# Optimization experiments

Hardware: AMD Instinct MI355X
Metric: run time of the kernel (lower is better)

The kernel has to match this reference:

```python
import jax, jax.numpy as jnp
import numpy as np

NUM_LOW, NUM_HIGH, DIM = 8192, 1024, 2048
EPS = 1e-10


def sparsemax(z):
    # z: [..., K]; Martins & Astudillo sparsemax along last axis.
    K = z.shape[-1]
    z_sorted = jnp.flip(jnp.sort(z, axis=-1), axis=-1)          # descending
    z_cum = jnp.cumsum(z_sorted, axis=-1)
    k = jnp.arange(1, K + 1, dtype=z.dtype)
    support = (1.0 + k * z_sorted) > z_cum                       # bool [..., K]
    k_sup = jnp.sum(support, axis=-1, keepdims=True)             # int [..., 1]
    tau = (jnp.take_along_axis(z_cum, k_sup - 1, axis=-1) - 1.0) / k_sup.astype(z.dtype)
    return jnp.maximum(z - tau, 0.0)


def normalize_rows(x, eps=EPS):
    return x / (jnp.sum(x, axis=1, keepdims=True) + eps)


def setup_inputs() -> dict:
    key = jax.random.key(0)
    k1, k2, k3, k4 = jax.random.split(key, 4)

    def xavier(k, shape):
        bound = float(np.sqrt(6.0 / (shape[0] + shape[1])))
        return jax.random.uniform(k, shape, jnp.float32, -bound, bound)

    return {
        "low_w": xavier(k1, (NUM_LOW, DIM)),    # low Concepts parameter
        "high_w": xavier(k2, (NUM_HIGH, DIM)),  # high Concepts parameter
        "Wq": xavier(k3, (DIM, DIM)),           # q_linear.weight (keep_head_dim, n_head=1)
        "Wk": xavier(k4, (DIM, DIM)),           # k_linear.weight
        "norm_low_concepts": 1,
        "norm_high_concepts": 1,
    }


def reference(low_w, high_w, Wq, Wk, norm_low_concepts, norm_high_concepts):
    # Concepts modules: return (possibly normalized) concepts + cosine similarity.
    low_normed = low_w / jnp.linalg.norm(low_w, axis=1, keepdims=True)
    low_concepts = low_normed if norm_low_concepts else low_w
    low_cos = low_normed @ low_normed.T                          # [NL, NL]

    high_normed = high_w / jnp.linalg.norm(high_w, axis=1, keepdims=True)
    high_concepts = high_normed if norm_high_concepts else high_w
    high_cos = high_normed @ high_normed.T                       # [NH, NH]

    # detach_low_concepts=True -> queries do not receive gradients
    low_q = jax.lax.stop_gradient(low_concepts)

    # ModifiedMultiHeadAttention (n_head=1, keep_head_dim -> d_head=DIM; eval mode,
    # so smooth_max is identity and sparsemax is deterministic).
    q = low_q @ Wq.T                                             # [NL, D]
    k = high_concepts @ Wk.T                                     # [NH, D]
    scale = 1.0 / jnp.sqrt(jnp.asarray(DIM, q.dtype))
    attn = sparsemax((q @ k.T) * scale)                          # [NL, NH]
    high_related_low = attn @ high_concepts                      # [NL, D]

    # output_high_concepts_type == "high_plus_low": add back aggregated low concepts
    aggregated_low = normalize_rows(attn.T) @ low_q              # [NH, D]
    output_high_concepts = high_related_low + attn @ aggregated_low  # [NL, D]

    return (low_concepts, low_cos, output_high_concepts, high_cos, attn)
```

## Files before the change

### kernel.cpp

```cpp
#include <hip/hip_runtime.h>
#include <hip/hip_bf16.h>
#include <stdint.h>

#define NL   8192
#define NHI  1024
#define DIMV 2048

typedef __attribute__((ext_vector_type(8))) short short8;
typedef __attribute__((ext_vector_type(4))) float f32x4;

__device__ __forceinline__ unsigned short f2bf(float x){
  unsigned u = __float_as_uint(x);
  u += 0x7FFFu + ((u >> 16) & 1u);
  return (unsigned short)(u >> 16);
}
__device__ __forceinline__ float bf2f(unsigned short b){
  return __uint_as_float(((unsigned)b) << 16);
}
__device__ __forceinline__ unsigned pack2bf(float a, float b){
  return (unsigned)f2bf(a) | ((unsigned)f2bf(b) << 16);
}

__device__ __forceinline__ void gload16(const void* g, void* l){
  __builtin_amdgcn_global_load_lds(
      (const __attribute__((address_space(1))) unsigned int*)g,
      (__attribute__((address_space(3))) unsigned int*)l, 16, 0, 0);
}

__global__ __launch_bounds__(256)
void prep_kernel(const float* __restrict__ low_w, const float* __restrict__ high_w,
                 const float* __restrict__ Wq, const float* __restrict__ Wk,
                 float* __restrict__ out_lowc, unsigned short* __restrict__ lowN,
                 unsigned short* __restrict__ highN,
                 unsigned short* __restrict__ WqB, unsigned short* __restrict__ WkB){
  int id = blockIdx.x;
  if(id < 9216){
    const float* W; float* oF; unsigned short* oB; int row;
    if(id < 8192){ W = low_w; oF = out_lowc; oB = lowN; row = id; }
    else         { W = high_w; oF = nullptr; oB = highN; row = id - 8192; }
    const float* r = W + (size_t)row * DIMV;
    int base = threadIdx.x * 8;
    float4 x0 = *(const float4*)(r + base);
    float4 x1 = *(const float4*)(r + base + 4);
    float ss = x0.x*x0.x + x0.y*x0.y + x0.z*x0.z + x0.w*x0.w
             + x1.x*x1.x + x1.y*x1.y + x1.z*x1.z + x1.w*x1.w;
    #pragma unroll
    for(int s = 1; s < 64; s <<= 1) ss += __shfl_xor(ss, s, 64);
    __shared__ float red[4];
    if((threadIdx.x & 63) == 0) red[threadIdx.x >> 6] = ss;
    __syncthreads();
    float tot = red[0] + red[1] + red[2] + red[3];
    float inv = 1.0f / sqrtf(tot);
    float y0=x0.x*inv, y1=x0.y*inv, y2=x0.z*inv, y3=x0.w*inv;
    float y4=x1.x*inv, y5=x1.y*inv, y6=x1.z*inv, y7=x1.w*inv;
    if(oF){
      float* o = oF + (size_t)row * DIMV + base;
      *(float4*)o       = make_float4(y0,y1,y2,y3);
      *(float4*)(o + 4) = make_float4(y4,y5,y6,y7);
    }
    uint4 u;
    u.x = pack2bf(y0,y1); u.y = pack2bf(y2,y3);
    u.z = pack2bf(y4,y5); u.w = pack2bf(y6,y7);
    *(uint4*)(oB + (size_t)row * DIMV + base) = u;
  } else {
    id -= 9216;
    const float* in; unsigned short* outp;
    if(id < 2048){ in = Wq; outp = WqB; } else { in = Wk; outp = WkB; id -= 2048; }
    size_t i = ((size_t)id * 256 + threadIdx.x) * 8;
    float4 x0 = *(const float4*)(in + i);
    float4 x1 = *(const float4*)(in + i + 4);
    uint4 u;
    u.x = pack2bf(x0.x,x0.y); u.y = pack2bf(x0.z,x0.w);
    u.z = pack2bf(x1.x,x1.y); u.w = pack2bf(x1.z,x1.w);
    *(uint4*)(outp + i) = u;
  }
}

template<int OUT_BF16, int MIRROR>
__global__ __launch_bounds__(256, 2)
void gemm_bt_kernel(const unsigned short* __restrict__ A,
                    const unsigned short* __restrict__ Bt,
                    float* __restrict__ Cf, unsigned short* __restrict__ Cb,
                    int M, int N, int K, float scale){
  __shared__ __align__(16) char smem[32768];
  unsigned short* sA = (unsigned short*)smem;
  unsigned short* sB = sA + 128 * 64;

  int tid = threadIdx.x, lane = tid & 63, wid = tid >> 6;
  int mBase, nBase;
  if(MIRROR){
    int orig = blockIdx.x;
    int id = (orig & 7) * 260 + (orig >> 3);
    int Si = 0, rem = id;
    for(;;){ int rl = 10 + 16*(15 - Si); if(rem < rl) break; rem -= rl; Si++; }
    int bi, bj;
    if(rem < 10){
      int ti = 0;
      while((ti+1)*4 - (((ti+1)*ti) >> 1) <= rem) ti++;
      int off = ti*4 - ((ti*(ti-1)) >> 1);
      int tj = ti + (rem - off);
      bi = Si*4 + ti; bj = Si*4 + tj;
    } else {
      int r2 = rem - 10;
      int Sj = Si + 1 + (r2 >> 4);
      int t = r2 & 15;
      bi = Si*4 + (t >> 2); bj = Sj*4 + (t & 3);
    }
    mBase = bi * 128; nBase = bj * 128;
  } else {
    int gx = gridDim.x, gy = gridDim.y;
    int nwg = gx * gy;
    int id = blockIdx.y * gx + blockIdx.x;
    if((nwg & 7) == 0){ int cpx = nwg >> 3; id = (id & 7) * cpx + (id >> 3); }
    mBase = (id / gx) * 128; nBase = (id % gx) * 128;
  }

  int chRow = lane >> 3;
  int chCol = (lane & 7) * 8;
  int wm = wid >> 1, wn = wid & 1;

  f32x4 acc[4][4];
  #pragma unroll
  for(int i=0;i<4;i++)
    #pragma unroll
    for(int j=0;j<4;j++) acc[i][j] = (f32x4){0.f,0.f,0.f,0.f};

  int kChunk = K / (int)gridDim.z;
  int kStart = kChunk * (int)blockIdx.z;
  if(!OUT_BF16) Cf += (size_t)blockIdx.z * M * N;

  for(int k0 = kStart; k0 < kStart + kChunk; k0 += 64){
    #pragma unroll
    for(int i = 0; i < 4; i++){
      int ch = wid * 4 + i;
      int arow = ch * 8 + chRow;
      gload16(A  + (size_t)(mBase + arow) * K + k0 + chCol, &sA[ch * 512]);
      gload16(Bt + (size_t)(nBase + arow) * K + k0 + chCol, &sB[ch * 512]);
    }
    __syncthreads();
    #pragma unroll
    for(int kk = 0; kk < 64; kk += 32){
      short8 a[4], b[4];
      int krd = kk + (lane >> 4) * 8;
      #pragma unroll
      for(int i = 0; i < 4; i++){
        int row = wm * 64 + i * 16 + (lane & 15);
        a[i] = *reinterpret_cast<const short8*>(&sA[row * 64 + krd]);
        int col = wn * 64 + i * 16 + (lane & 15);
        b[i] = *reinterpret_cast<const short8*>(&sB[col * 64 + krd]);
      }
      #pragma unroll
      for(int i = 0; i < 4; i++)
        #pragma unroll
        for(int j = 0; j < 4; j++)
          acc[i][j] = __builtin_amdgcn_mfma_f32_16x16x32_bf16(a[i], b[j], acc[i][j], 0, 0, 0);
    }
    __syncthreads();
  }

  #pragma unroll
  for(int i = 0; i < 4; i++){
    #pragma unroll
    for(int j = 0; j < 4; j++){
      int row = mBase + wm * 64 + i * 16 + (lane >> 4) * 4;
      int col = nBase + wn * 64 + j * 16 + (lane & 15);
      #pragma unroll
      for(int r = 0; r < 4; r++){
        float v = acc[i][j][r] * scale;
        size_t off = (size_t)(row + r) * N + col;
        if(OUT_BF16) Cb[off] = f2bf(v);
        else         Cf[off] = v;
      }
    }
  }

  if(MIRROR && mBase != nBase){
    float* tf = (float*)smem;
    #pragma unroll
    for(int rq = 0; rq < 4; rq++){
      int qm = rq >> 1, qn = rq & 1;
      __syncthreads();
      if(wm == qm && wn == qn){
        #pragma unroll
        for(int i = 0; i < 4; i++)
          #pragma unroll
          for(int j = 0; j < 4; j++){
            int rl = i * 16 + (lane >> 4) * 4;
            int cl = j * 16 + (lane & 15);
            #pragma unroll
            for(int r = 0; r < 4; r++)
              tf[(rl + r) * 65 + cl] = acc[i][j][r] * scale;
          }
      }
      __syncthreads();
      int mr = tid >> 2, seg = tid & 3;
      size_t obase = (size_t)(nBase + qn * 64 + mr) * N + mBase + qm * 64 + seg * 16;
      #pragma unroll
      for(int k4 = 0; k4 < 4; k4++){
        float4 v;
        v.x = tf[(seg * 16 + k4 * 4 + 0) * 65 + mr];
        v.y = tf[(seg * 16 + k4 * 4 + 1) * 65 + mr];
        v.z = tf[(seg * 16 + k4 * 4 + 2) * 65 + mr];
        v.w = tf[(seg * 16 + k4 * 4 + 3) * 65 + mr];
        *(float4*)(Cf + obase + k4 * 4) = v;
      }
    }
  }
}

__global__ __launch_bounds__(256)
void combine2_kernel(const float* __restrict__ hcPart, float* __restrict__ out_highcos,
                     const float* __restrict__ kPart, unsigned short* __restrict__ kB){
  int id = blockIdx.x;
  if(id < 512){
    size_t i = ((size_t)id * 256 + threadIdx.x) * 8;
    float4 a0 = *(const float4*)(hcPart + i);
    float4 a1 = *(const float4*)(hcPart + i + 4);
    float4 b0 = *(const float4*)(hcPart + 1048576 + i);
    float4 b1 = *(const float4*)(hcPart + 1048576 + i + 4);
    *(float4*)(out_highcos + i)     = make_float4(a0.x+b0.x, a0.y+b0.y, a0.z+b0.z, a0.w+b0.w);
    *(float4*)(out_highcos + i + 4) = make_float4(a1.x+b1.x, a1.y+b1.y, a1.z+b1.z, a1.w+b1.w);
  } else {
    size_t i = ((size_t)(id - 512) * 256 + threadIdx.x) * 8;
    float4 a0 = *(const float4*)(kPart + i);
    float4 a1 = *(const float4*)(kPart + i + 4);
    float4 b0 = *(const float4*)(kPart + 2097152 + i);
    float4 b1 = *(const float4*)(kPart + 2097152 + i + 4);
    uint4 u;
    u.x = pack2bf(a0.x+b0.x, a0.y+b0.y); u.y = pack2bf(a0.z+b0.z, a0.w+b0.w);
    u.z = pack2bf(a1.x+b1.x, a1.y+b1.y); u.w = pack2bf(a1.z+b1.z, a1.w+b1.w);
    *(uint4*)(kB + i) = u;
  }
}

__global__ __launch_bounds__(256)
void sparsemax_kernel(float* __restrict__ S, unsigned short* __restrict__ attnBf){
  int wid = threadIdx.x >> 6, lane = threadIdx.x & 63;
  int row = blockIdx.x * 4 + wid;
  float* z = S + (size_t)row * NHI;
  float v[16];
  #pragma unroll
  for(int j = 0; j < 16; j++) v[j] = z[j * 64 + lane];
  float mx = v[0];
  #pragma unroll
  for(int j = 1; j < 16; j++) mx = fmaxf(mx, v[j]);
  #pragma unroll
  for(int s = 1; s < 64; s <<= 1) mx = fmaxf(mx, __shfl_xor(mx, s, 64));
  float lo = mx - 1.0f, hi = mx;
  for(int it = 0; it < 40; it++){
    float mid = 0.5f * (lo + hi);
    float sum = 0.f;
    #pragma unroll
    for(int j = 0; j < 16; j++) sum += fmaxf(v[j] - mid, 0.f);
    #pragma unroll
    for(int s = 1; s < 64; s <<= 1) sum += __shfl_xor(sum, s, 64);
    if(sum >= 1.0f) lo = mid; else hi = mid;
  }
  float cnt = 0.f, ssum = 0.f;
  #pragma unroll
  for(int j = 0; j < 16; j++){
    if(v[j] > lo){ cnt += 1.f; ssum += v[j]; }
  }
  #pragma unroll
  for(int s = 1; s < 64; s <<= 1){
    cnt  += __shfl_xor(cnt,  s, 64);
    ssum += __shfl_xor(ssum, s, 64);
  }
  float tau = (ssum - 1.0f) / cnt;
  #pragma unroll
  for(int j = 0; j < 16; j++){
    float a = fmaxf(v[j] - tau, 0.f);
    z[j * 64 + lane] = a;
    attnBf[(size_t)row * NHI + j * 64 + lane] = f2bf(a);
  }
}

__global__ __launch_bounds__(256)
void colsum_part_kernel(const float* __restrict__ attn, float* __restrict__ part){
  int chunk = blockIdx.x;
  int t = threadIdx.x;
  const float* p = attn + (size_t)chunk * 32 * NHI;
  float a0=0,a1=0,a2=0,a3=0;
  for(int r = 0; r < 32; r++){
    a0 += p[(size_t)r*NHI + t];
    a1 += p[(size_t)r*NHI + t + 256];
    a2 += p[(size_t)r*NHI + t + 512];
    a3 += p[(size_t)r*NHI + t + 768];
  }
  float* q = part + (size_t)chunk * NHI;
  q[t]=a0; q[t+256]=a1; q[t+512]=a2; q[t+768]=a3;
}
__global__ __launch_bounds__(256)
void colsum_final_kernel(const float* __restrict__ part, float* __restrict__ colsum){
  int c = blockIdx.x * 256 + threadIdx.x;
  float s = 0.f;
  for(int i = 0; i < 256; i++) s += part[(size_t)i * NHI + c];
  colsum[c] = s;
}

__global__ __launch_bounds__(256)
void transpose3_kernel(const unsigned short* __restrict__ attnB, unsigned short* __restrict__ attnT,
                       const unsigned short* __restrict__ lowN,  unsigned short* __restrict__ lowNT,
                       const unsigned short* __restrict__ highN, unsigned short* __restrict__ highNT){
  __shared__ unsigned short tile[64][65];
  int id = blockIdx.x;
  const unsigned short* in; unsigned short* out; int R, C, tx, ty;
  if(id < 2048){        in = attnB; out = attnT;  R = NL;  C = NHI;  tx = id & 15; ty = id >> 4; }
  else if(id < 6144){ id -= 2048;
                        in = lowN;  out = lowNT;  R = NL;  C = DIMV; tx = id & 31; ty = id >> 5; }
  else {              id -= 6144;
                        in = highN; out = highNT; R = NHI; C = DIMV; tx = id & 31; ty = id >> 5; }
  int c0 = tx * 64, r0 = ty * 64;
  int t = threadIdx.x;
  int ci = t & 63, r4 = t >> 6;
  #pragma unroll
  for(int k = 0; k < 16; k++){
    int r = k * 4 + r4;
    tile[r][ci] = in[(size_t)(r0 + r) * C + c0 + ci];
  }
  __syncthreads();
  #pragma unroll
  for(int k = 0; k < 16; k++){
    int cc = k * 4 + r4;
    out[(size_t)(c0 + cc) * R + r0 + ci] = tile[ci][cc];
  }
}

__global__ __launch_bounds__(256)
void mt_kernel(const unsigned short* __restrict__ highNT, const float* __restrict__ aggP,
               const float* __restrict__ colsum, unsigned short* __restrict__ Mt){
  int idx = blockIdx.x * 256 + threadIdx.x;
  int h = idx & 1023;
  float s = aggP[idx] + aggP[idx + 2097152];
  float val = bf2f(highNT[idx]) + s / (colsum[h] + 1e-10f);
  Mt[idx] = f2bf(val);
}

extern "C" void kernel_launch(void* const* d_in, const int* in_sizes, int n_in,
                              void* d_out, int out_size, void* d_ws, size_t ws_size,
                              hipStream_t stream){
  const float* low_w  = (const float*)d_in[0];
  const float* high_w = (const float*)d_in[1];
  const float* Wq     = (const float*)d_in[2];
  const float* Wk     = (const float*)d_in[3];
  float* out = (float*)d_out;

  char* ws = (char*)d_ws;
  unsigned short* lowN  = (unsigned short*)(ws);
  float*          aggP  = (float*)(ws);
  unsigned short* highN = (unsigned short*)(ws + 33554432);
  unsigned short* WqB   = (unsigned short*)(ws + 37748736);
  unsigned short* WkB   = (unsigned short*)(ws + 46137344);
  unsigned short* attnB = (unsigned short*)(ws + 37748736);
  unsigned short* qB    = (unsigned short*)(ws + 54525952);
  unsigned short* lowNT = qB;
  unsigned short* kB    = (unsigned short*)(ws + 88080384);
  float*          part  = (float*)(ws + 88080384);
  float*          colsum= (float*)(ws + 88080384 + 1048576);
  unsigned short* attnT = (unsigned short*)(ws + 92274688);
  float*          kPart = (float*)(ws + 92274688);
  unsigned short* Mt    = (unsigned short*)(ws + 109051904);
  unsigned short* highNT= (unsigned short*)(ws + 113246208);
  float*          hcPart= (float*)(ws + 109051904);

  float* out_lowc    = out;
  float* out_lowcos  = out + 16777216;
  float* out_high    = out + 83886080;
  float* out_highcos = out + 100663296;
  float* out_attn    = out + 101711872;

  const float scl = 1.0f / sqrtf((float)DIMV);

  prep_kernel<<<13312, 256, 0, stream>>>(low_w, high_w, Wq, Wk,
                                         out_lowc, lowN, highN, WqB, WkB);
  gemm_bt_kernel<0,1><<<2080, 256, 0, stream>>>(lowN, lowN, out_lowcos, nullptr,
                                                NL, NL, DIMV, 1.0f);
  gemm_bt_kernel<0,0><<<dim3(8,8,2), 256, 0, stream>>>(highN, highN, hcPart, nullptr,
                                                       NHI, NHI, DIMV, 1.0f);
  gemm_bt_kernel<0,0><<<dim3(16,8,2), 256, 0, stream>>>(highN, WkB, kPart, nullptr,
                                                        NHI, DIMV, DIMV, 1.0f);
  combine2_kernel<<<1536, 256, 0, stream>>>(hcPart, out_highcos, kPart, kB);
  gemm_bt_kernel<1,0><<<dim3(16,64), 256, 0, stream>>>(lowN, WqB, nullptr, qB,
                                                       NL, DIMV, DIMV, 1.0f);
  gemm_bt_kernel<0,0><<<dim3(8,64), 256, 0, stream>>>(qB, kB, out_attn, nullptr,
                                                      NL, NHI, DIMV, scl);
  sparsemax_kernel<<<NL/4, 256, 0, stream>>>(out_attn, attnB);
  colsum_part_kernel<<<256, 256, 0, stream>>>(out_attn, part);
  colsum_final_kernel<<<4, 256, 0, stream>>>(part, colsum);
  transpose3_kernel<<<6656, 256, 0, stream>>>(attnB, attnT, lowN, lowNT, highN, highNT);
  gemm_bt_kernel<0,0><<<dim3(8,16,2), 256, 0, stream>>>(lowNT, attnT, aggP, nullptr,
                                                        DIMV, NHI, NL, 1.0f);
  mt_kernel<<<8192, 256, 0, stream>>>(highNT, aggP, colsum, Mt);
  gemm_bt_kernel<0,0><<<dim3(16,64), 256, 0, stream>>>(attnB, Mt, out_high, nullptr,
                                                       NL, DIMV, NHI, 1.0f);
}
```

Measured before the change: 628.7 us.

## Reassociate attention logits via Wq^T Wk product to skip the large Q projection

Computes scores as lowN·(highN·(Wq^T Wk)^T)^T instead of projecting all 8192 low concepts through Wq. It first forms G = Wq^T·Wk (2048^3), then R2 = highN·G^T (1024x2048x2048), then a single NL x NHI x DIM GEMM. This removes the 8192x2048x2048 Q projection and the split-K K projection and combine, and adds a transposing cast kernel for the weights. The extra bf16 rounding of G and R2 changes numerics slightly.

Measured after the change: 612.3 us. -2.6%, faster.

```diff
diff --git a/kernel.cpp b/kernel.cpp
--- a/kernel.cpp
+++ b/kernel.cpp
@@ -29,50 +29,59 @@
 
 __global__ __launch_bounds__(256)
 void prep_kernel(const float* __restrict__ low_w, const float* __restrict__ high_w,
-                 const float* __restrict__ Wq, const float* __restrict__ Wk,
                  float* __restrict__ out_lowc, unsigned short* __restrict__ lowN,
-                 unsigned short* __restrict__ highN,
-                 unsigned short* __restrict__ WqB, unsigned short* __restrict__ WkB){
+                 unsigned short* __restrict__ highN){
   int id = blockIdx.x;
-  if(id < 9216){
-    const float* W; float* oF; unsigned short* oB; int row;
-    if(id < 8192){ W = low_w; oF = out_lowc; oB = lowN; row = id; }
-    else         { W = high_w; oF = nullptr; oB = highN; row = id - 8192; }
-    const float* r = W + (size_t)row * DIMV;
-    int base = threadIdx.x * 8;
-    float4 x0 = *(const float4*)(r + base);
-    float4 x1 = *(const float4*)(r + base + 4);
-    float ss = x0.x*x0.x + x0.y*x0.y + x0.z*x0.z + x0.w*x0.w
-             + x1.x*x1.x + x1.y*x1.y + x1.z*x1.z + x1.w*x1.w;
-    #pragma unroll
-    for(int s = 1; s < 64; s <<= 1) ss += __shfl_xor(ss, s, 64);
-    __shared__ float red[4];
-    if((threadIdx.x & 63) == 0) red[threadIdx.x >> 6] = ss;
-    __syncthreads();
-    float tot = red[0] + red[1] + red[2] + red[3];
-    float inv = 1.0f / sqrtf(tot);
-    float y0=x0.x*inv, y1=x0.y*inv, y2=x0.z*inv, y3=x0.w*inv;
-    float y4=x1.x*inv, y5=x1.y*inv, y6=x1.z*inv, y7=x1.w*inv;
-    if(oF){
-      float* o = oF + (size_t)row * DIMV + base;
-      *(float4*)o       = make_float4(y0,y1,y2,y3);
-      *(float4*)(o + 4) = make_float4(y4,y5,y6,y7);
-    }
-    uint4 u;
-    u.x = pack2bf(y0,y1); u.y = pack2bf(y2,y3);
-    u.z = pack2bf(y4,y5); u.w = pack2bf(y6,y7);
-    *(uint4*)(oB + (size_t)row * DIMV + base) = u;
-  } else {
-    id -= 9216;
-    const float* in; unsigned short* outp;
-    if(id < 2048){ in = Wq; outp = WqB; } else { in = Wk; outp = WkB; id -= 2048; }
-    size_t i = ((size_t)id * 256 + threadIdx.x) * 8;
-    float4 x0 = *(const float4*)(in + i);
-    float4 x1 = *(const float4*)(in + i + 4);
-    uint4 u;
-    u.x = pack2bf(x0.x,x0.y); u.y = pack2bf(x0.z,x0.w);
-    u.z = pack2bf(x1.x,x1.y); u.w = pack2bf(x1.z,x1.w);
-    *(uint4*)(outp + i) = u;
+  const float* W; float* oF; unsigned short* oB; int row;
+  if(id < 8192){ W = low_w; oF = out_lowc; oB = lowN; row = id; }
+  else         { W = high_w; oF = nullptr; oB = highN; row = id - 8192; }
+  const float* r = W + (size_t)row * DIMV;
+  int base = threadIdx.x * 8;
+  float4 x0 = *(const float4*)(r + base);
+  float4 x1 = *(const float4*)(r + base + 4);
+  float ss = x0.x*x0.x + x0.y*x0.y + x0.z*x0.z + x0.w*x0.w
+           + x1.x*x1.x + x1.y*x1.y + x1.z*x1.z + x1.w*x1.w;
+  #pragma unroll
+  for(int s = 1; s < 64; s <<= 1) ss += __shfl_xor(ss, s, 64);
+  __shared__ float red[4];
+  if((threadIdx.x & 63) == 0) red[threadIdx.x >> 6] = ss;
+  __syncthreads();
+  float tot = red[0] + red[1] + red[2] + red[3];
+  float inv = 1.0f / sqrtf(tot);
+  float y0=x0.x*inv, y1=x0.y*inv, y2=x0.z*inv, y3=x0.w*inv;
+  float y4=x1.x*inv, y5=x1.y*inv, y6=x1.z*inv, y7=x1.w*inv;
+  if(oF){
+    float* o = oF + (size_t)row * DIMV + base;
+    *(float4*)o       = make_float4(y0,y1,y2,y3);
+    *(float4*)(o + 4) = make_float4(y4,y5,y6,y7);
+  }
+  uint4 u;
+  u.x = pack2bf(y0,y1); u.y = pack2bf(y2,y3);
+  u.z = pack2bf(y4,y5); u.w = pack2bf(y6,y7);
+  *(uint4*)(oB + (size_t)row * DIMV + base) = u;
+}
+
+__global__ __launch_bounds__(256)
+void castT_kernel(const float* __restrict__ Wq, unsigned short* __restrict__ WqT,
+                  const float* __restrict__ Wk, unsigned short* __restrict__ WkT){
+  __shared__ unsigned short tile[64][65];
+  int id = blockIdx.x;
+  const float* in; unsigned short* outp;
+  if(id < 1024){ in = Wq; outp = WqT; } else { in = Wk; outp = WkT; id -= 1024; }
+  int tx = id & 31, ty = id >> 5;
+  int c0 = tx * 64, r0 = ty * 64;
+  int t = threadIdx.x;
+  int ci = t & 63, r4 = t >> 6;
+  #pragma unroll
+  for(int k = 0; k < 16; k++){
+    int r = k * 4 + r4;
+    tile[r][ci] = f2bf(in[(size_t)(r0 + r) * 2048 + c0 + ci]);
+  }
+  __syncthreads();
+  #pragma unroll
+  for(int k = 0; k < 16; k++){
+    int cc = k * 4 + r4;
+    outp[(size_t)(c0 + cc) * 2048 + r0 + ci] = tile[ci][cc];
   }
 }
 
@@ -209,28 +218,14 @@
 }
 
 __global__ __launch_bounds__(256)
-void combine2_kernel(const float* __restrict__ hcPart, float* __restrict__ out_highcos,
-                     const float* __restrict__ kPart, unsigned short* __restrict__ kB){
-  int id = blockIdx.x;
-  if(id < 512){
-    size_t i = ((size_t)id * 256 + threadIdx.x) * 8;
-    float4 a0 = *(const float4*)(hcPart + i);
-    float4 a1 = *(const float4*)(hcPart + i + 4);
-    float4 b0 = *(const float4*)(hcPart + 1048576 + i);
-    float4 b1 = *(const float4*)(hcPart + 1048576 + i + 4);
-    *(float4*)(out_highcos + i)     = make_float4(a0.x+b0.x, a0.y+b0.y, a0.z+b0.z, a0.w+b0.w);
-    *(float4*)(out_highcos + i + 4) = make_float4(a1.x+b1.x, a1.y+b1.y, a1.z+b1.z, a1.w+b1.w);
-  } else {
-    size_t i = ((size_t)(id - 512) * 256 + threadIdx.x) * 8;
-    float4 a0 = *(const float4*)(kPart + i);
-    float4 a1 = *(const float4*)(kPart + i + 4);
-    float4 b0 = *(const float4*)(kPart + 2097152 + i);
-    float4 b1 = *(const float4*)(kPart + 2097152 + i + 4);
-    uint4 u;
-    u.x = pack2bf(a0.x+b0.x, a0.y+b0.y); u.y = pack2bf(a0.z+b0.z, a0.w+b0.w);
-    u.z = pack2bf(a1.x+b1.x, a1.y+b1.y); u.w = pack2bf(a1.z+b1.z, a1.w+b1.w);
-    *(uint4*)(kB + i) = u;
-  }
+void combine_hc_kernel(const float* __restrict__ hcPart, float* __restrict__ out_highcos){
+  size_t i = ((size_t)blockIdx.x * 256 + threadIdx.x) * 8;
+  float4 a0 = *(const float4*)(hcPart + i);
+  float4 a1 = *(const float4*)(hcPart + i + 4);
+  float4 b0 = *(const float4*)(hcPart + 1048576 + i);
+  float4 b1 = *(const float4*)(hcPart + 1048576 + i + 4);
+  *(float4*)(out_highcos + i)     = make_float4(a0.x+b0.x, a0.y+b0.y, a0.z+b0.z, a0.w+b0.w);
+  *(float4*)(out_highcos + i + 4) = make_float4(a1.x+b1.x, a1.y+b1.y, a1.z+b1.z, a1.w+b1.w);
 }
 
 __global__ __launch_bounds__(256)
@@ -349,19 +344,18 @@
   unsigned short* lowN  = (unsigned short*)(ws);
   float*          aggP  = (float*)(ws);
   unsigned short* highN = (unsigned short*)(ws + 33554432);
-  unsigned short* WqB   = (unsigned short*)(ws + 37748736);
-  unsigned short* WkB   = (unsigned short*)(ws + 46137344);
+  unsigned short* WqT   = (unsigned short*)(ws + 37748736);
+  unsigned short* WkT   = (unsigned short*)(ws + 46137344);
   unsigned short* attnB = (unsigned short*)(ws + 37748736);
-  unsigned short* qB    = (unsigned short*)(ws + 54525952);
-  unsigned short* lowNT = qB;
-  unsigned short* kB    = (unsigned short*)(ws + 88080384);
+  unsigned short* G     = (unsigned short*)(ws + 54525952);
+  unsigned short* R2t   = (unsigned short*)(ws + 62914560);
+  unsigned short* lowNT = (unsigned short*)(ws + 54525952);
   float*          part  = (float*)(ws + 88080384);
   float*          colsum= (float*)(ws + 88080384 + 1048576);
   unsigned short* attnT = (unsigned short*)(ws + 92274688);
-  float*          kPart = (float*)(ws + 92274688);
+  float*          hcPart= (float*)(ws + 109051904);
   unsigned short* Mt    = (unsigned short*)(ws + 109051904);
   unsigned short* highNT= (unsigned short*)(ws + 113246208);
-  float*          hcPart= (float*)(ws + 109051904);
 
   float* out_lowc    = out;
   float* out_lowcos  = out + 16777216;
@@ -371,18 +365,18 @@
 
   const float scl = 1.0f / sqrtf((float)DIMV);
 
-  prep_kernel<<<13312, 256, 0, stream>>>(low_w, high_w, Wq, Wk,
-                                         out_lowc, lowN, highN, WqB, WkB);
+  prep_kernel<<<9216, 256, 0, stream>>>(low_w, high_w, out_lowc, lowN, highN);
+  castT_kernel<<<2048, 256, 0, stream>>>(Wq, WqT, Wk, WkT);
   gemm_bt_kernel<0,1><<<2080, 256, 0, stream>>>(lowN, lowN, out_lowcos, nullptr,
                                                 NL, NL, DIMV, 1.0f);
+  gemm_bt_kernel<1,0><<<dim3(16,16), 256, 0, stream>>>(WqT, WkT, nullptr, G,
+                                                       DIMV, DIMV, DIMV, 1.0f);
   gemm_bt_kernel<0,0><<<dim3(8,8,2), 256, 0, stream>>>(highN, highN, hcPart, nullptr,
                                                        NHI, NHI, DIMV, 1.0f);
-  gemm_bt_kernel<0,0><<<dim3(16,8,2), 256, 0, stream>>>(highN, WkB, kPart, nullptr,
-                                                        NHI, DIMV, DIMV, 1.0f);
-  combine2_kernel<<<1536, 256, 0, stream>>>(hcPart, out_highcos, kPart, kB);
-  gemm_bt_kernel<1,0><<<dim3(16,64), 256, 0, stream>>>(lowN, WqB, nullptr, qB,
-                                                       NL, DIMV, DIMV, 1.0f);
-  gemm_bt_kernel<0,0><<<dim3(8,64), 256, 0, stream>>>(qB, kB, out_attn, nullptr,
+  combine_hc_kernel<<<512, 256, 0, stream>>>(hcPart, out_highcos);
+  gemm_bt_kernel<1,0><<<dim3(16,8), 256, 0, stream>>>(highN, G, nullptr, R2t,
+                                                      NHI, DIMV, DIMV, 1.0f);
+  gemm_bt_kernel<0,0><<<dim3(8,64), 256, 0, stream>>>(lowN, R2t, out_attn, nullptr,
                                                       NL, NHI, DIMV, scl);
   sparsemax_kernel<<<NL/4, 256, 0, stream>>>(out_attn, attnB);
   colsum_part_kernel<<<256, 256, 0, stream>>>(out_attn, part);
```
